# Kernel optimization log

Measured on AMD Instinct MI355X. Metric: run time of the kernel, lower is better.

The kernel has to match this reference:

```python
import jax, jax.numpy as jnp
import numpy as np

EPS = 1e-6
KH, KW = 3, 3
SH, SW = 1, 1


def _unfold(x, kh, kw, sh, sw):
    # x: [N, C, H, W] -> patches [N, C, kh*kw, L], L = ox*oy (torch.nn.Unfold layout)
    N, C, H, W = x.shape
    ox = (H - kh) // sh + 1
    oy = (W - kw) // sw + 1
    pats = [x[:, :, i:i + sh * ox:sh, j:j + sw * oy:sw]
            for i in range(kh) for j in range(kw)]
    p = jnp.stack(pats, axis=2)  # [N, C, K, ox, oy]
    return p.reshape(N, C, kh * kw, ox * oy), ox, oy


def setup_inputs() -> dict:
    key = jax.random.key(0)
    kx, k1, k2 = jax.random.split(key, 3)
    x = jax.random.uniform(kx, (32, 2, 64, 64, 64), dtype=jnp.float32)
    w1 = jax.random.uniform(k1, (64, KH * KW), dtype=jnp.float32)
    w2 = jax.random.uniform(k2, (128, 64), dtype=jnp.float32)
    return {"x": x, "w1": w1, "w2": w2}


def reference(x, w1, w2):
    B = x.shape[0]
    out_ch = w2.shape[0]
    xr = x[:, 0]  # rotation plane [B, C, H, W]
    xa = x[:, 1]  # magnitude plane

    pr, ox, oy = _unfold(xr, KH, KW, SH, SW)  # [B, C, K, L]
    pa, _, _ = _unfold(xa, KH, KW, SH, SW)

    # weightNormalize1: squared weights normalized by GLOBAL sum (rot branch)
    w1_glob = w1 ** 2 / jnp.sum(w1 ** 2)
    w2_glob = w2 ** 2 / jnp.sum(w2 ** 2)
    # weightNormalize (drop_prob=0): squared weights normalized PER ROW (abs branch)
    w1_row = w1 ** 2 / jnp.sum(w1 ** 2, axis=1, keepdims=True)
    w2_row = w2 ** 2 / jnp.sum(w2 ** 2, axis=1, keepdims=True)

    # rotation branch: two weighted contractions
    rot = jnp.einsum('bckl,ck->bcl', pr, w1_glob)          # [B, C, L]
    out_rot = jnp.einsum('bcl,oc->bol', rot, w2_glob)      # [B, O, L]
    out_rot = out_rot.reshape(B, 1, out_ch, ox, oy)

    # magnitude branch: log -> weighted contractions -> exp
    la = jnp.log(pa + EPS)                                  # [B, C, K, L]
    a1 = jnp.einsum('bckl,ck->bcl', la, w1_row)             # [B, C, L]
    out_abs = jnp.exp(jnp.einsum('bcl,oc->bol', a1, w2_row))
    out_abs = out_abs.reshape(B, 1, out_ch, ox, oy)

    return jnp.concatenate([out_rot, out_abs], axis=1)  # [B, 2, O, ox, oy]
```

## Files before the change

### kernel.cpp

```cpp
#include <hip/hip_runtime.h>
#include <cstdint>
#include <cstddef>

#define EPSF 1e-6f

typedef __attribute__((ext_vector_type(4))) float f32x4;
typedef __attribute__((ext_vector_type(8))) short s16x8;
typedef union { s16x8 v; unsigned u[4]; } s16x8u;

static __device__ __forceinline__ void pack2(float a, float b, unsigned& H, unsigned& L) {
    unsigned h, l;
    asm("v_cvt_pk_bf16_f32 %0, %1, %2" : "=v"(h) : "v"(a), "v"(b));
    float ra = a - __uint_as_float(h << 16);
    float rb = b - __uint_as_float(h & 0xffff0000u);
    asm("v_cvt_pk_bf16_f32 %0, %1, %2" : "=v"(l) : "v"(ra), "v"(rb));
    H = h; L = l;
}
static __device__ __forceinline__ unsigned packH(float a, float b) {
    unsigned h;
    asm("v_cvt_pk_bf16_f32 %0, %1, %2" : "=v"(h) : "v"(a), "v"(b));
    return h;
}


__global__ __launch_bounds__(256) void prep(const float* __restrict__ w1,
                                            const float* __restrict__ w2,
                                            float* __restrict__ ws) {
    __shared__ float s1row[64];
    __shared__ float red[4];
    __shared__ float rs8[8];
    const int t = threadIdx.x;
    const int lane = t & 63;
    const int wv = t >> 6;
    const int gid = blockIdx.x * 256 + t;

    float s = 0.f;
    #pragma unroll
    for (int i = 0; i < 32; ++i) { float v = w2[t + 256 * i]; s += v * v; }
    #pragma unroll
    for (int d = 32; d > 0; d >>= 1) s += __shfl_xor(s, d);
    if (lane == 0) red[wv] = s;

    if (t < 64) {
        float rs = 0.f;
        #pragma unroll
        for (int k = 0; k < 9; ++k) { float v = w1[t * 9 + k]; rs += v * v; }
        s1row[t] = rs;
    }

    if (blockIdx.x < 16) {
        const int r8 = t >> 5;
        const int e = t & 31;
        const int row = blockIdx.x * 8 + r8;
        float v0 = w2[row * 64 + e];
        float v1 = w2[row * 64 + 32 + e];
        float rr = v0 * v0 + v1 * v1;
        #pragma unroll
        for (int d = 16; d > 0; d >>= 1) rr += __shfl_down(rr, d);
        if (e == 0) rs8[r8] = rr;
    }
    __syncthreads();

    const float t2 = red[0] + red[1] + red[2] + red[3];
    float a = s1row[lane];
    #pragma unroll
    for (int d = 32; d > 0; d >>= 1) a += __shfl_xor(a, d);
    const float t1 = a;

    unsigned* wsu = (unsigned*)ws;
    if (gid < 4096) {
        const int row = gid >> 5;
        const int cp = gid & 31;
        float v0 = w2[row * 64 + 2 * cp];
        float v1 = w2[row * 64 + 2 * cp + 1];
        float q0 = v0 * v0, q1 = v1 * v1;
        const float rs = rs8[t >> 5];
        unsigned H, L;
        pack2(q0 / t2, q1 / t2, H, L);
        wsu[1152 + row * 32 + cp] = H;
        wsu[5248 + row * 32 + cp] = L;
        pack2(q0 / rs, q1 / rs, H, L);
        wsu[9344 + row * 32 + cp] = H;
        wsu[13440 + row * 32 + cp] = L;
    } else if (gid < 4672) {
        const int i = gid - 4096;
        const int c = i / 9;
        const int k = i - c * 9;
        float v = w1[i];
        float q = v * v;
        ws[c * 9 + k] = q / t1;
        ws[576 + c * 9 + k] = q / s1row[c];
    }
}

__global__ __launch_bounds__(512) void conv_fused(const float* __restrict__ x,
                                                  const float* __restrict__ ws,
                                                  float* __restrict__ out) {
    const int b = blockIdx.x;
    const int branch = blockIdx.y;
    const int hg = blockIdx.z;
    const int h0 = hg * 2;
    const int t = threadIdx.x;
    const int lane = t & 63;
    const int w = __builtin_amdgcn_readfirstlane(t >> 6);
    const int lm = lane & 15;
    const int q = lane >> 4;
    const bool dual = (branch != 0);

    __shared__ unsigned rotH[128 * 33];
    __shared__ unsigned rotL[128 * 33];

    const float* __restrict__ w1n = ws + branch * 576;
    const unsigned* __restrict__ wsu = (const unsigned*)ws;
    const unsigned* __restrict__ w2H = wsu + 1152 + branch * 8192;
    const unsigned* __restrict__ w2L = w2H + 4096;
    const float* __restrict__ xb = x + (size_t)(b * 2 + branch) * (64 * 4096);

    const int cpair = w * 4 + q;
    const int c0 = 2 * cpair;
    const int oc0 = w * 16;

    const float* xp = xb + c0 * 4096 + h0 * 64;
    const int x0 = 4 * lm;
    const int xe = (lm < 15) ? x0 + 4 : 60;
    float pa[2][4], pb[2][4];

    {
        float4 va[4]; float2 ea[4];
        #pragma unroll
        for (int r = 0; r < 4; ++r) va[r] = *(const float4*)(xp + r * 64 + x0);
        #pragma unroll
        for (int r = 0; r < 4; ++r) ea[r] = *(const float2*)(xp + r * 64 + xe);

        const float* wc0 = w1n + c0 * 9;
        if (dual) {
            #pragma unroll
            for (int r = 0; r < 4; ++r) {
                va[r].x = __logf(va[r].x + EPSF); va[r].y = __logf(va[r].y + EPSF);
                va[r].z = __logf(va[r].z + EPSF); va[r].w = __logf(va[r].w + EPSF);
                ea[r].x = __logf(ea[r].x + EPSF); ea[r].y = __logf(ea[r].y + EPSF);
            }
        }
        #pragma unroll
        for (int row = 0; row < 2; ++row) {
            #pragma unroll
            for (int rr = 0; rr < 3; ++rr) {
                const float4 u = va[row + rr];
                const float e0 = ea[row + rr].x, e1 = ea[row + rr].y;
                const float t0 = wc0[rr * 3], t1_ = wc0[rr * 3 + 1], t2_ = wc0[rr * 3 + 2];
                if (rr == 0) {
                    pa[row][0] = u.x * t0 + u.y * t1_ + u.z * t2_;
                    pa[row][1] = u.y * t0 + u.z * t1_ + u.w * t2_;
                    pa[row][2] = u.z * t0 + u.w * t1_ + e0 * t2_;
                    pa[row][3] = u.w * t0 + e0 * t1_ + e1 * t2_;
                } else {
                    pa[row][0] += u.x * t0 + u.y * t1_ + u.z * t2_;
                    pa[row][1] += u.y * t0 + u.z * t1_ + u.w * t2_;
                    pa[row][2] += u.z * t0 + u.w * t1_ + e0 * t2_;
                    pa[row][3] += u.w * t0 + e0 * t1_ + e1 * t2_;
                }
            }
        }
    }

    {
        float4 vb[4]; float2 eb[4];
        #pragma unroll
        for (int r = 0; r < 4; ++r) vb[r] = *(const float4*)(xp + 4096 + r * 64 + x0);
        #pragma unroll
        for (int r = 0; r < 4; ++r) eb[r] = *(const float2*)(xp + 4096 + r * 64 + xe);

        const float* wc1 = w1n + c0 * 9 + 9;
        if (dual) {
            #pragma unroll
            for (int r = 0; r < 4; ++r) {
                vb[r].x = __logf(vb[r].x + EPSF); vb[r].y = __logf(vb[r].y + EPSF);
                vb[r].z = __logf(vb[r].z + EPSF); vb[r].w = __logf(vb[r].w + EPSF);
                eb[r].x = __logf(eb[r].x + EPSF); eb[r].y = __logf(eb[r].y + EPSF);
            }
        }
        #pragma unroll
        for (int row = 0; row < 2; ++row) {
            #pragma unroll
            for (int rr = 0; rr < 3; ++rr) {
                const float4 u = vb[row + rr];
                const float e0 = eb[row + rr].x, e1 = eb[row + rr].y;
                const float t0 = wc1[rr * 3], t1_ = wc1[rr * 3 + 1], t2_ = wc1[rr * 3 + 2];
                if (rr == 0) {
                    pb[row][0] = u.x * t0 + u.y * t1_ + u.z * t2_;
                    pb[row][1] = u.y * t0 + u.z * t1_ + u.w * t2_;
                    pb[row][2] = u.z * t0 + u.w * t1_ + e0 * t2_;
                    pb[row][3] = u.w * t0 + e0 * t1_ + e1 * t2_;
                } else {
                    pb[row][0] += u.x * t0 + u.y * t1_ + u.z * t2_;
                    pb[row][1] += u.y * t0 + u.z * t1_ + u.w * t2_;
                    pb[row][2] += u.z * t0 + u.w * t1_ + e0 * t2_;
                    pb[row][3] += u.w * t0 + e0 * t1_ + e1 * t2_;
                }
            }
        }
    }

    #pragma unroll
    for (int row = 0; row < 2; ++row) {
        #pragma unroll
        for (int i = 0; i < 4; ++i) {
            const int pxl = row * 64 + 4 * lm + i;
            if (dual) {
                unsigned H, L;
                pack2(pa[row][i], pb[row][i], H, L);
                rotH[pxl * 33 + cpair] = H;
                rotL[pxl * 33 + cpair] = L;
            } else {
                rotH[pxl * 33 + cpair] = packH(pa[row][i], pb[row][i]);
            }
        }
    }

    s16x8u aH[2], aL[2];
    #pragma unroll
    for (int kk = 0; kk < 2; ++kk) {
        const int off = (oc0 + lm) * 32 + kk * 16 + q * 4;
        #pragma unroll
        for (int j = 0; j < 4; ++j) aH[kk].u[j] = w2H[off + j];
    }
    if (dual) {
        #pragma unroll
        for (int kk = 0; kk < 2; ++kk) {
            const int off = (oc0 + lm) * 32 + kk * 16 + q * 4;
            #pragma unroll
            for (int j = 0; j < 4; ++j) aL[kk].u[j] = w2L[off + j];
        }
    }
    __syncthreads();

    const int ocr = oc0 + q * 4;
    #pragma unroll
    for (int g = 0; g < 2; ++g) {
        f32x4 acc[4];
        #pragma unroll
        for (int ntl = 0; ntl < 4; ++ntl) acc[ntl] = (f32x4){0.f, 0.f, 0.f, 0.f};

        __builtin_amdgcn_s_setprio(1);
        if (dual) {
            #pragma unroll
            for (int ntl = 0; ntl < 4; ++ntl) {
                #pragma unroll
                for (int kk = 0; kk < 2; ++kk) {
                    const int idx = ((g * 4 + ntl) * 16 + lm) * 33 + kk * 16 + q * 4;
                    s16x8u bH, bL;
                    #pragma unroll
                    for (int j = 0; j < 4; ++j) bH.u[j] = rotH[idx + j];
                    #pragma unroll
                    for (int j = 0; j < 4; ++j) bL.u[j] = rotL[idx + j];
                    acc[ntl] = __builtin_amdgcn_mfma_f32_16x16x32_bf16(aH[kk].v, bH.v, acc[ntl], 0, 0, 0);
                    acc[ntl] = __builtin_amdgcn_mfma_f32_16x16x32_bf16(aH[kk].v, bL.v, acc[ntl], 0, 0, 0);
                    acc[ntl] = __builtin_amdgcn_mfma_f32_16x16x32_bf16(aL[kk].v, bH.v, acc[ntl], 0, 0, 0);
                }
            }
        } else {
            #pragma unroll
            for (int ntl = 0; ntl < 4; ++ntl) {
                #pragma unroll
                for (int kk = 0; kk < 2; ++kk) {
                    const int idx = ((g * 4 + ntl) * 16 + lm) * 33 + kk * 16 + q * 4;
                    s16x8u bH;
                    #pragma unroll
                    for (int j = 0; j < 4; ++j) bH.u[j] = rotH[idx + j];
                    acc[ntl] = __builtin_amdgcn_mfma_f32_16x16x32_bf16(aH[kk].v, bH.v, acc[ntl], 0, 0, 0);
                }
            }
        }
        __builtin_amdgcn_s_setprio(0);

        #pragma unroll
        for (int ntl = 0; ntl < 4; ++ntl) {
            const int col = ntl * 16 + lm;
            if (col < 62) {
                const size_t base =
                    ((size_t)((b * 2 + branch) * 128 + ocr)) * 3844 +
                    (size_t)(h0 + g) * 62 + col;
                #pragma unroll
                for (int r = 0; r < 4; ++r) {
                    float v = acc[ntl][r];
                    if (dual) v = __expf(v);
                    out[base + (size_t)r * 3844] = v;
                }
            }
        }
    }
}

extern "C" void kernel_launch(void* const* d_in, const int* in_sizes, int n_in,
                              void* d_out, int out_size, void* d_ws, size_t ws_size,
                              hipStream_t stream) {
    const float* x  = (const float*)d_in[0];
    const float* w1 = (const float*)d_in[1];
    const float* w2 = (const float*)d_in[2];
    float* out = (float*)d_out;
    float* ws  = (float*)d_ws;

    prep<<<19, 256, 0, stream>>>(w1, w2, ws);

    dim3 grid(32, 2, 31);
    conv_fused<<<grid, 512, 0, stream>>>(x, ws, out);
}
```

Baseline: 203.1 us.

## Split fused conv into pack kernel writing MFMA fragments and separate GEMM kernel

Splits the fused kernel in two. The first computes the depthwise 3x3 stage and writes bf16 hi/lo values to global workspace, already laid out as MFMA B-fragments. The second kernel reads those fragments with vector loads, runs the 1x1 channel-mix GEMM and applies exp. This removes the LDS staging, the __syncthreads and the shared-memory occupancy limit, and allows a larger grid for the GEMM stage. In exchange it adds a global round trip for the intermediate (tens of MB for hi plus lo) and an extra kernel launch.

```diff
diff --git a/kernel.cpp b/kernel.cpp
--- a/kernel.cpp
+++ b/kernel.cpp
@@ -7,6 +7,10 @@
 typedef __attribute__((ext_vector_type(4))) float f32x4;
 typedef __attribute__((ext_vector_type(8))) short s16x8;
 typedef union { s16x8 v; unsigned u[4]; } s16x8u;
+
+#define OFF_H 32768
+#define FRAG_N (64 * 248 * 2 * 256)
+#define OFF_L (OFF_H + FRAG_N)
 
 static __device__ __forceinline__ void pack2(float a, float b, unsigned& H, unsigned& L) {
     unsigned h, l;
@@ -93,36 +97,29 @@
     }
 }
 
-__global__ __launch_bounds__(512) void conv_fused(const float* __restrict__ x,
-                                                  const float* __restrict__ ws,
-                                                  float* __restrict__ out) {
+__global__ __launch_bounds__(512) void conv_pack(const float* __restrict__ x,
+                                                 const float* __restrict__ ws,
+                                                 float* __restrict__ wso) {
     const int b = blockIdx.x;
     const int branch = blockIdx.y;
     const int hg = blockIdx.z;
     const int h0 = hg * 2;
     const int t = threadIdx.x;
     const int lane = t & 63;
-    const int w = __builtin_amdgcn_readfirstlane(t >> 6);
+    const int w = t >> 6;
     const int lm = lane & 15;
     const int q = lane >> 4;
     const bool dual = (branch != 0);
 
-    __shared__ unsigned rotH[128 * 33];
-    __shared__ unsigned rotL[128 * 33];
-
     const float* __restrict__ w1n = ws + branch * 576;
-    const unsigned* __restrict__ wsu = (const unsigned*)ws;
-    const unsigned* __restrict__ w2H = wsu + 1152 + branch * 8192;
-    const unsigned* __restrict__ w2L = w2H + 4096;
     const float* __restrict__ xb = x + (size_t)(b * 2 + branch) * (64 * 4096);
 
     const int cpair = w * 4 + q;
     const int c0 = 2 * cpair;
-    const int oc0 = w * 16;
-
     const float* xp = xb + c0 * 4096 + h0 * 64;
     const int x0 = 4 * lm;
     const int xe = (lm < 15) ? x0 + 4 : 60;
+
     float pa[2][4], pb[2][4];
 
     {
@@ -162,7 +159,6 @@
             }
         }
     }
-
     {
         float4 vb[4]; float2 eb[4];
         #pragma unroll
@@ -201,91 +197,114 @@
         }
     }
 
+    unsigned* __restrict__ wsu = (unsigned*)wso;
+    const int bb = b * 2 + branch;
+    const int kk = cpair >> 4;
+    const int qd = (cpair >> 2) & 3;
+    const int j  = cpair & 3;
+    const int ct = lm >> 2;
+    const int lf0 = (lm & 3) * 4;
     #pragma unroll
     for (int row = 0; row < 2; ++row) {
+        const int tile = (h0 + row) * 4 + ct;
+        const unsigned blk = (((unsigned)(bb * 248 + tile)) * 2 + kk) * 256 + qd * 64 + lf0 * 4 + j;
         #pragma unroll
         for (int i = 0; i < 4; ++i) {
-            const int pxl = row * 64 + 4 * lm + i;
             if (dual) {
                 unsigned H, L;
                 pack2(pa[row][i], pb[row][i], H, L);
-                rotH[pxl * 33 + cpair] = H;
-                rotL[pxl * 33 + cpair] = L;
+                wsu[OFF_H + blk + i * 4] = H;
+                wsu[OFF_L + blk + i * 4] = L;
             } else {
-                rotH[pxl * 33 + cpair] = packH(pa[row][i], pb[row][i]);
-            }
-        }
-    }
+                wsu[OFF_H + blk + i * 4] = packH(pa[row][i], pb[row][i]);
+            }
+        }
+    }
+}
+
+__global__ __launch_bounds__(512) void gemm_out(const float* __restrict__ ws,
+                                                float* __restrict__ out) {
+    const int b = blockIdx.x;
+    const int branch = blockIdx.y;
+    const int row = blockIdx.z;
+    const int t = threadIdx.x;
+    const int lane = t & 63;
+    const int w = __builtin_amdgcn_readfirstlane(t >> 6);
+    const int lm = lane & 15;
+    const int q = lane >> 4;
+    const bool dual = (branch != 0);
+    const int bb = b * 2 + branch;
+
+    const unsigned* __restrict__ wsu = (const unsigned*)ws;
+    const unsigned* __restrict__ w2H = wsu + 1152 + branch * 8192;
+    const unsigned* __restrict__ w2L = w2H + 4096;
+
+    const int oc0 = w * 16;
 
     s16x8u aH[2], aL[2];
     #pragma unroll
     for (int kk = 0; kk < 2; ++kk) {
         const int off = (oc0 + lm) * 32 + kk * 16 + q * 4;
         #pragma unroll
-        for (int j = 0; j < 4; ++j) aH[kk].u[j] = w2H[off + j];
+        for (int jj = 0; jj < 4; ++jj) aH[kk].u[jj] = w2H[off + jj];
     }
     if (dual) {
         #pragma unroll
         for (int kk = 0; kk < 2; ++kk) {
             const int off = (oc0 + lm) * 32 + kk * 16 + q * 4;
             #pragma unroll
-            for (int j = 0; j < 4; ++j) aL[kk].u[j] = w2L[off + j];
-        }
-    }
-    __syncthreads();
+            for (int jj = 0; jj < 4; ++jj) aL[kk].u[jj] = w2L[off + jj];
+        }
+    }
+
+    const unsigned rowbase = (unsigned)(bb * 248 + row * 4);
+
+    f32x4 acc[4];
+    #pragma unroll
+    for (int nt = 0; nt < 4; ++nt) acc[nt] = (f32x4){0.f, 0.f, 0.f, 0.f};
+
+    if (dual) {
+        #pragma unroll
+        for (int nt = 0; nt < 4; ++nt) {
+            #pragma unroll
+            for (int kk = 0; kk < 2; ++kk) {
+                const unsigned fb = ((rowbase + nt) * 2 + kk) * 256 + lane * 4;
+                s16x8u bH, bL;
+                #pragma unroll
+                for (int jj = 0; jj < 4; ++jj) bH.u[jj] = wsu[OFF_H + fb + jj];
+                #pragma unroll
+                for (int jj = 0; jj < 4; ++jj) bL.u[jj] = wsu[OFF_L + fb + jj];
+                acc[nt] = __builtin_amdgcn_mfma_f32_16x16x32_bf16(aH[kk].v, bH.v, acc[nt], 0, 0, 0);
+                acc[nt] = __builtin_amdgcn_mfma_f32_16x16x32_bf16(aH[kk].v, bL.v, acc[nt], 0, 0, 0);
+                acc[nt] = __builtin_amdgcn_mfma_f32_16x16x32_bf16(aL[kk].v, bH.v, acc[nt], 0, 0, 0);
+            }
+        }
+    } else {
+        #pragma unroll
+        for (int nt = 0; nt < 4; ++nt) {
+            #pragma unroll
+            for (int kk = 0; kk < 2; ++kk) {
+                const unsigned fb = ((rowbase + nt) * 2 + kk) * 256 + lane * 4;
+                s16x8u bH;
+                #pragma unroll
+                for (int jj = 0; jj < 4; ++jj) bH.u[jj] = wsu[OFF_H + fb + jj];
+                acc[nt] = __builtin_amdgcn_mfma_f32_16x16x32_bf16(aH[kk].v, bH.v, acc[nt], 0, 0, 0);
+            }
+        }
+    }
 
     const int ocr = oc0 + q * 4;
     #pragma unroll
-    for (int g = 0; g < 2; ++g) {
-        f32x4 acc[4];
-        #pragma unroll
-        for (int ntl = 0; ntl < 4; ++ntl) acc[ntl] = (f32x4){0.f, 0.f, 0.f, 0.f};
-
-        __builtin_amdgcn_s_setprio(1);
-        if (dual) {
-            #pragma unroll
-            for (int ntl = 0; ntl < 4; ++ntl) {
-                #pragma unroll
-                for (int kk = 0; kk < 2; ++kk) {
-                    const int idx = ((g * 4 + ntl) * 16 + lm) * 33 + kk * 16 + q * 4;
-                    s16x8u bH, bL;
-                    #pragma unroll
-                    for (int j = 0; j < 4; ++j) bH.u[j] = rotH[idx + j];
-                    #pragma unroll
-                    for (int j = 0; j < 4; ++j) bL.u[j] = rotL[idx + j];
-                    acc[ntl] = __builtin_amdgcn_mfma_f32_16x16x32_bf16(aH[kk].v, bH.v, acc[ntl], 0, 0, 0);
-                    acc[ntl] = __builtin_amdgcn_mfma_f32_16x16x32_bf16(aH[kk].v, bL.v, acc[ntl], 0, 0, 0);
-                    acc[ntl] = __builtin_amdgcn_mfma_f32_16x16x32_bf16(aL[kk].v, bH.v, acc[ntl], 0, 0, 0);
-                }
-            }
-        } else {
-            #pragma unroll
-            for (int ntl = 0; ntl < 4; ++ntl) {
-                #pragma unroll
-                for (int kk = 0; kk < 2; ++kk) {
-                    const int idx = ((g * 4 + ntl) * 16 + lm) * 33 + kk * 16 + q * 4;
-                    s16x8u bH;
-                    #pragma unroll
-                    for (int j = 0; j < 4; ++j) bH.u[j] = rotH[idx + j];
-                    acc[ntl] = __builtin_amdgcn_mfma_f32_16x16x32_bf16(aH[kk].v, bH.v, acc[ntl], 0, 0, 0);
-                }
-            }
-        }
-        __builtin_amdgcn_s_setprio(0);
-
-        #pragma unroll
-        for (int ntl = 0; ntl < 4; ++ntl) {
-            const int col = ntl * 16 + lm;
-            if (col < 62) {
-                const size_t base =
-                    ((size_t)((b * 2 + branch) * 128 + ocr)) * 3844 +
-                    (size_t)(h0 + g) * 62 + col;
-                #pragma unroll
-                for (int r = 0; r < 4; ++r) {
-                    float v = acc[ntl][r];
-                    if (dual) v = __expf(v);
-                    out[base + (size_t)r * 3844] = v;
-                }
+    for (int nt = 0; nt < 4; ++nt) {
+        const int col = nt * 16 + lm;
+        if (col < 62) {
+            const size_t base =
+                ((size_t)(bb * 128 + ocr)) * 3844 + (size_t)row * 62 + col;
+            #pragma unroll
+            for (int r = 0; r < 4; ++r) {
+                float v = acc[nt][r];
+                if (dual) v = __expf(v);
+                out[base + (size_t)r * 3844] = v;
             }
         }
     }
@@ -302,6 +321,9 @@
 
     prep<<<19, 256, 0, stream>>>(w1, w2, ws);
 
-    dim3 grid(32, 2, 31);
-    conv_fused<<<grid, 512, 0, stream>>>(x, ws, out);
-}
+    dim3 gA(32, 2, 31);
+    conv_pack<<<gA, 512, 0, stream>>>(x, ws, ws);
+
+    dim3 gB(32, 2, 62);
+    gemm_out<<<gB, 512, 0, stream>>>(ws, out);
+}
```

Measured after the change: 252.6 us. 24.3% more time.
